# Kernel tuning notes

Measured on AMD Instinct MI355X. Metric: run time of the kernel, lower is better.

Reference implementation:

```python
import jax, jax.numpy as jnp
import numpy as np
import math

B, T, HID = 4, 1024, 1024
N_ATTN, N_HEAD, CTX = 1024, 64, 1024
HEAD_SIZE = N_ATTN // N_HEAD


def _make_time_w():
    ww = np.ones((N_HEAD, CTX), dtype=np.float32)
    curve = np.arange(CTX, dtype=np.float64) - (CTX - 1)  # -(CTX-1-i)
    for h in range(N_HEAD):
        decay = math.pow(CTX, -(h + 1) / (N_HEAD - 1)) if h < N_HEAD - 1 else 0.0
        ww[h] = np.exp(curve * decay).astype(np.float32)
    return jnp.asarray(ww)


def setup_inputs() -> dict:
    key = jax.random.key(0)
    ks = jax.random.split(key, 9)
    s = 0.02
    return {
        'x': jax.random.normal(ks[0], (B, T, HID), jnp.float32),
        'time_w': _make_time_w(),                                   # [H, CTX]
        'time_alpha': jnp.ones((N_HEAD, 1, CTX), jnp.float32),
        'time_beta': jnp.ones((N_HEAD, CTX, 1), jnp.float32),
        'time_gamma': jnp.ones((CTX, 1), jnp.float32),
        'Wk': jax.random.normal(ks[1], (HID, N_ATTN), jnp.float32) * s,
        'bk': jnp.zeros((N_ATTN,), jnp.float32),
        'Wv': jax.random.normal(ks[2], (HID, N_ATTN), jnp.float32) * s,
        'bv': jnp.zeros((N_ATTN,), jnp.float32),
        'Wr': jax.random.normal(ks[3], (HID, N_ATTN), jnp.float32) * s,
        'br': jnp.zeros((N_ATTN,), jnp.float32),
        'Wo': jax.random.normal(ks[4], (N_ATTN, HID), jnp.float32) * s,
        'bo': jnp.zeros((HID,), jnp.float32),
    }


def reference(x, time_w, time_alpha, time_beta, time_gamma, Wk, bk, Wv, bv, Wr, br, Wo, bo):
    Bn, Tn, C = x.shape
    H, TT = time_w.shape
    hs = N_ATTN // H
    # --- Toeplitz causal decay matrix: w[h,t,u] = time_w[h, TT-1-(t-u)] for u<=t else 0 ---
    t = jnp.arange(Tn)
    rel = (TT - 1) - t[:, None] + t[None, :]            # [T, T]
    mask = t[None, :] <= t[:, None]                     # u <= t (causal)
    w = jnp.where(mask[None], time_w[:, jnp.clip(rel, 0, TT - 1)], 0.0)  # [H, T, T]
    w = w * time_alpha[:, :, :Tn] * time_beta[:, :Tn, :]
    # --- half-channel time shift (shift first C//2 channels back by one step) ---
    half = x[:, :, : C // 2]
    shifted = jnp.concatenate([jnp.zeros_like(half[:, :1]), half[:, :-1]], axis=1)
    xs = jnp.concatenate([shifted, x[:, :, C // 2:]], axis=-1)
    # --- projections ---
    k = xs @ Wk + bk
    v = xs @ Wv + bv
    r = xs @ Wr + br
    k = jnp.exp(jnp.clip(k, -60.0, 30.0))
    sum_k = jnp.cumsum(k, axis=1)
    kv = (k * v).reshape(Bn, Tn, H, hs)
    wkv = jnp.einsum('htu,buhc->bthc', w, kv).reshape(Bn, Tn, -1)
    rwkv = jax.nn.sigmoid(r) * wkv / sum_k
    out = rwkv @ Wo + bo
    return out * time_gamma[:Tn]
```

## Files before the change

### kernel.cpp

```cpp
#include <hip/hip_runtime.h>
#include <hip/hip_bf16.h>
#include <cstddef>
#include <cstdint>

#define Bn   4
#define Tn   1024
#define HID  1024
#define NH   64
#define HS   16
#define NA   1024

typedef short v8s __attribute__((ext_vector_type(8)));
typedef float v4f __attribute__((ext_vector_type(4)));

typedef __attribute__((address_space(1))) void* as1_void;
typedef __attribute__((address_space(3))) void* as3_void;

__device__ __forceinline__ void gload_lds16(const void* g, void* l) {
    __builtin_amdgcn_global_load_lds((as1_void)(void*)g, (as3_void)l, 16, 0, 0);
}

__device__ __forceinline__ short f2bf(float f) {
    __hip_bfloat16 h = __float2bfloat16(f);
    return *reinterpret_cast<short*>(&h);
}
__device__ __forceinline__ float bf2f(short s) {
    __hip_bfloat16 h = *reinterpret_cast<__hip_bfloat16*>(&s);
    return __bfloat162float(h);
}

__global__ __launch_bounds__(256)
void prep(const float* __restrict__ x,
          const float* __restrict__ W0, const float* __restrict__ W1,
          const float* __restrict__ W2, const float* __restrict__ W3,
          short* __restrict__ xs, short* __restrict__ Wt)
{
    __shared__ float tile[32][33];
    const int bid = blockIdx.x;
    const int tid = threadIdx.x;
    if (bid < 4096) {
        int idx = bid * 256 + tid;
        int m  = idx >> 8;
        int c4 = (idx & 255) * 4;
        int t  = m & (Tn - 1);
        float4 v;
        if (c4 < HID / 2) {
            if (t == 0) v = make_float4(0.f, 0.f, 0.f, 0.f);
            else        v = *(const float4*)(x + (size_t)(m - 1) * HID + c4);
        } else {
            v = *(const float4*)(x + (size_t)m * HID + c4);
        }
        short4 o;
        o.x = f2bf(v.x); o.y = f2bf(v.y); o.z = f2bf(v.z); o.w = f2bf(v.w);
        *(short4*)(xs + (size_t)m * HID + c4) = o;
    } else {
        int b2 = bid - 4096;
        int z  = b2 >> 10;
        int rem = b2 & 1023;
        const float* W = (z == 0) ? W0 : (z == 1) ? W1 : (z == 2) ? W2 : W3;
        short* dst = Wt + (size_t)z * 1024 * 1024;
        int k0 = (rem & 31) * 32;
        int n0 = (rem >> 5) * 32;
        int tx = tid & 31;
        int ty = tid >> 5;
        #pragma unroll
        for (int j = 0; j < 4; ++j)
            tile[ty + 8 * j][tx] = W[(size_t)(k0 + ty + 8 * j) * NA + n0 + tx];
        __syncthreads();
        #pragma unroll
        for (int j = 0; j < 4; ++j)
            dst[(size_t)(n0 + ty + 8 * j) * HID + k0 + tx] = f2bf(tile[tx][ty + 8 * j]);
    }
}

template<int EPI, int TN>
__global__ __launch_bounds__(256)
void gemm_db(const short* __restrict__ A, const short* __restrict__ Bt,
             const float* __restrict__ b0, const float* __restrict__ b1,
             const float* __restrict__ b2,
             short* __restrict__ kout, short* __restrict__ vout,
             short* __restrict__ sout, float* __restrict__ fout,
             const float* __restrict__ gamma)
{
    constexpr int NT = TN / 32;
    constexpr int BI = TN / 64;
    constexpr int STAGE = 2 * 128 * 32 + 2 * TN * 32;
    constexpr int TILE  = (EPI == 0) ? 128 * 136 : 0;
    constexpr int SMEM  = STAGE > TILE ? STAGE : TILE;
    __shared__ short smem[SMEM];
    short* As = smem;
    short* Bs = smem + 2 * 128 * 32;

    const int tid  = threadIdx.x;
    const int wave = tid >> 6;
    const int lane = tid & 63;

    int id = blockIdx.x;
    int brow, bcol;
    if (TN == 128) { int grp = id / 192, l = id % 192; brow = grp * 8 + (l & 7); bcol = (l >> 3) % 24; }
    else           { int grp = id / 128, l = id % 128; brow = grp * 8 + (l & 7); bcol = l >> 3; }
    const int bm = brow * 128;
    const int bn = bcol * TN;

    const int wm = (wave & 1) * 64;
    const int wn = (wave >> 1) * (TN / 2);
    const int lm = lane & 15;
    const int lq = lane >> 4;
    const int lr = lane >> 2;
    const int l4 = lane & 3;

    v4f acc[4][NT];
    #pragma unroll
    for (int i = 0; i < 4; ++i)
        #pragma unroll
        for (int j = 0; j < NT; ++j) acc[i][j] = (v4f){0.f, 0.f, 0.f, 0.f};

    const short* ag[2];
    int adst[2];
    #pragma unroll
    for (int i = 0; i < 2; ++i) {
        int r = wave * 32 + i * 16 + lr;
        int q = (l4 - (r >> 1)) & 3;
        ag[i]  = A + (size_t)(bm + r) * 1024 + q * 8;
        adst[i] = (wave * 32 + i * 16) * 32;
    }
    const short* bg[BI];
    int bdst[BI];
    #pragma unroll
    for (int i = 0; i < BI; ++i) {
        int r = wave * (TN / 4) + i * 16 + lr;
        int q = (l4 - (r >> 1)) & 3;
        bg[i]  = Bt + (size_t)(bn + r) * 1024 + q * 8;
        bdst[i] = (wave * (TN / 4) + i * 16) * 32;
    }
    int afo[4], bfo[NT];
    #pragma unroll
    for (int t = 0; t < 4; ++t) {
        int r = wm + t * 16 + lm;
        afo[t] = r * 32 + (((lq + (r >> 1)) & 3)) * 8;
    }
    #pragma unroll
    for (int nt = 0; nt < NT; ++nt) {
        int r = wn + nt * 16 + lm;
        bfo[nt] = r * 32 + (((lq + (r >> 1)) & 3)) * 8;
    }

    #pragma unroll
    for (int i = 0; i < 2; ++i)  gload_lds16(ag[i],  &As[adst[i]]);
    #pragma unroll
    for (int i = 0; i < BI; ++i) gload_lds16(bg[i],  &Bs[bdst[i]]);

    #pragma unroll 2
    for (int it = 0; it < 32; ++it) {
        const int cur = it & 1;
        if (it < 31) {
            int k1 = (it + 1) * 32;
            int nxt = cur ^ 1;
            #pragma unroll
            for (int i = 0; i < 2; ++i)
                gload_lds16(ag[i] + k1, &As[nxt * 4096 + adst[i]]);
            #pragma unroll
            for (int i = 0; i < BI; ++i)
                gload_lds16(bg[i] + k1, &Bs[nxt * TN * 32 + bdst[i]]);
            asm volatile("s_waitcnt vmcnt(%0)" :: "i"(2 + BI) : "memory");
        } else {
            asm volatile("s_waitcnt vmcnt(0)" ::: "memory");
        }
        asm volatile("s_barrier" ::: "memory");

        v8s af[4], bfr[NT];
        #pragma unroll
        for (int t = 0; t < 4; ++t)
            af[t] = *(const v8s*)&As[cur * 4096 + afo[t]];
        #pragma unroll
        for (int nt = 0; nt < NT; ++nt)
            bfr[nt] = *(const v8s*)&Bs[cur * TN * 32 + bfo[nt]];
        #pragma unroll
        for (int mt = 0; mt < 4; ++mt)
            #pragma unroll
            for (int nt = 0; nt < NT; ++nt)
                acc[mt][nt] = __builtin_amdgcn_mfma_f32_16x16x32_bf16(
                    bfr[nt], af[mt], acc[mt][nt], 0, 0, 0);

        asm volatile("s_barrier" ::: "memory");
    }

    if (EPI == 0) {
        __syncthreads();
        short* tile = smem;
        const int type = bn >> 10;
        const int cb = bn & 1023;
        const float* bias = (type == 0) ? b0 : (type == 1) ? b1 : b2;
        #pragma unroll
        for (int mt = 0; mt < 4; ++mt) {
            int ml = wm + mt * 16 + lm;
            #pragma unroll
            for (int nt = 0; nt < NT; ++nt) {
                int nl = wn + nt * 16 + lq * 4;
                float4 bv4 = *(const float4*)&bias[cb + nl];
                short4 o;
                #pragma unroll
                for (int r = 0; r < 4; ++r) {
                    float v = acc[mt][nt][r] + ((const float*)&bv4)[r];
                    if (type == 0) {
                        v = fminf(fmaxf(v, -60.f), 30.f);
                        v = __expf(v);
                    } else if (type == 2) {
                        v = __builtin_amdgcn_rcpf(1.f + __expf(-v));
                    }
                    ((short*)&o)[r] = f2bf(v);
                }
                *(short4*)&tile[ml * 136 + nl] = o;
            }
        }
        __syncthreads();
        short* outp = (type == 0) ? kout : (type == 1) ? vout : sout;
        const int rml = tid >> 4;
        const int rnl = (tid & 15) * 8;
        #pragma unroll
        for (int p = 0; p < 8; ++p) {
            int ml = p * 16 + rml;
            int4 d = *(const int4*)&tile[ml * 136 + rnl];
            *(int4*)&outp[(size_t)(bm + ml) * 1024 + cb + rnl] = d;
        }
    } else {
        #pragma unroll
        for (int mt = 0; mt < 4; ++mt) {
            int m = bm + wm + mt * 16 + lm;
            float g = gamma[m & (Tn - 1)];
            #pragma unroll
            for (int nt = 0; nt < NT; ++nt) {
                int n0 = bn + wn + nt * 16 + lq * 4;
                float4 bv4 = *(const float4*)&b0[n0];
                float4 o;
                o.x = (acc[mt][nt][0] + bv4.x) * g;
                o.y = (acc[mt][nt][1] + bv4.y) * g;
                o.z = (acc[mt][nt][2] + bv4.z) * g;
                o.w = (acc[mt][nt][3] + bv4.w) * g;
                *(float4*)&fout[(size_t)m * 1024 + n0] = o;
            }
        }
    }
}

#define SEG 16
#define SEGL 64

__global__ __launch_bounds__(256)
void scan_passA(const short* __restrict__ kexp, const short* __restrict__ vbuf,
                const float* __restrict__ time_w, const float* __restrict__ alpha,
                float2* __restrict__ states)
{
    int gid = blockIdx.x * 256 + threadIdx.x;
    int c2  = (gid & 511) * 2;
    int b   = (gid >> 9) & 3;
    int seg = gid >> 11;
    int h   = c2 >> 4;
    float r = time_w[h * Tn + (Tn - 2)];
    int t0 = seg * SEGL;
    size_t base = ((size_t)(b * Tn + t0)) * NA + c2;
    const float* ap = alpha + h * Tn + t0;
    float S0 = 0.f, S1 = 0.f, ks0 = 0.f, ks1 = 0.f;
    #pragma unroll 4
    for (int i = 0; i < SEGL; ++i) {
        short2 kk = *(const short2*)(kexp + base + (size_t)i * NA);
        short2 vv = *(const short2*)(vbuf + base + (size_t)i * NA);
        float ke0 = bf2f(kk.x), ke1 = bf2f(kk.y);
        float a = ap[i];
        S0 = S0 * r + ke0 * bf2f(vv.x) * a;
        S1 = S1 * r + ke1 * bf2f(vv.y) * a;
        ks0 += ke0; ks1 += ke1;
    }
    int sidx = seg * 4096 + b * 1024 + c2;
    *(float4*)&states[sidx] = make_float4(S0, ks0, S1, ks1);
}

__global__ __launch_bounds__(256)
void scan_passC(const short* __restrict__ kexp, const short* __restrict__ vbuf,
                const short* __restrict__ sigr,
                const float* __restrict__ time_w, const float* __restrict__ alpha,
                const float* __restrict__ beta,
                const float2* __restrict__ states, short* __restrict__ out)
{
    int gid = blockIdx.x * 256 + threadIdx.x;
    int c2  = (gid & 511) * 2;
    int b   = (gid >> 9) & 3;
    int seg = gid >> 11;
    int h   = c2 >> 4;
    float r = time_w[h * Tn + (Tn - 2)];
    float rp = r;
    #pragma unroll
    for (int i = 0; i < 6; ++i) rp = rp * rp;
    float S0 = 0.f, ks0 = 0.f, S1 = 0.f, ks1 = 0.f;
    for (int s = 0; s < seg; ++s) {
        float2 st0 = states[s * 4096 + b * 1024 + c2];
        float2 st1 = states[s * 4096 + b * 1024 + c2 + 1];
        S0 = S0 * rp + st0.x;  ks0 += st0.y;
        S1 = S1 * rp + st1.x;  ks1 += st1.y;
    }
    int t0 = seg * SEGL;
    size_t base = ((size_t)(b * Tn + t0)) * NA + c2;
    const float* ap = alpha + h * Tn + t0;
    const float* bp = beta  + h * Tn + t0;
    #pragma unroll 4
    for (int i = 0; i < SEGL; ++i) {
        size_t idx = base + (size_t)i * NA;
        short2 kk = *(const short2*)(kexp + idx);
        short2 vv = *(const short2*)(vbuf + idx);
        short2 ss = *(const short2*)(sigr + idx);
        float a = ap[i], bt = bp[i];
        float ke0 = bf2f(kk.x), ke1 = bf2f(kk.y);
        S0 = S0 * r + ke0 * bf2f(vv.x) * a;
        S1 = S1 * r + ke1 * bf2f(vv.y) * a;
        ks0 += ke0; ks1 += ke1;
        short2 o;
        o.x = f2bf(bf2f(ss.x) * bt * S0 * __builtin_amdgcn_rcpf(ks0));
        o.y = f2bf(bf2f(ss.y) * bt * S1 * __builtin_amdgcn_rcpf(ks1));
        *(short2*)(out + idx) = o;
    }
}

extern "C" void kernel_launch(void* const* d_in, const int* in_sizes, int n_in,
                              void* d_out, int out_size, void* d_ws, size_t ws_size,
                              hipStream_t stream)
{
    const float* x      = (const float*)d_in[0];
    const float* time_w = (const float*)d_in[1];
    const float* alpha  = (const float*)d_in[2];
    const float* beta   = (const float*)d_in[3];
    const float* gamma  = (const float*)d_in[4];
    const float* Wk     = (const float*)d_in[5];
    const float* bk     = (const float*)d_in[6];
    const float* Wv     = (const float*)d_in[7];
    const float* bv     = (const float*)d_in[8];
    const float* Wr     = (const float*)d_in[9];
    const float* br     = (const float*)d_in[10];
    const float* Wo     = (const float*)d_in[11];
    const float* bo     = (const float*)d_in[12];
    float* out = (float*)d_out;

    char* ws = (char*)d_ws;

    short*  kbuf  = (short*)(ws);
    short*  vbuf  = (short*)(ws + ( 8u << 20));
    short*  sbuf  = (short*)(ws + (16u << 20));
    short*  xsbuf = (short*)(ws + (24u << 20));
    short*  Wt    = (short*)(ws + (32u << 20));
    float2* states= (float2*)(ws + (40u << 20));

    dim3 thr(256);

    prep<<<dim3(8192), thr, 0, stream>>>(x, Wk, Wv, Wr, Wo, xsbuf, Wt);

    gemm_db<0, 128><<<dim3(768), thr, 0, stream>>>(
        xsbuf, Wt, bk, bv, br, kbuf, vbuf, sbuf, nullptr, nullptr);

    scan_passA<<<dim3(128), thr, 0, stream>>>(kbuf, vbuf, time_w, alpha, states);
    scan_passC<<<dim3(128), thr, 0, stream>>>(kbuf, vbuf, sbuf,
                                              time_w, alpha, beta, states, xsbuf);

    gemm_db<1, 64><<<dim3(512), thr, 0, stream>>>(
        xsbuf, Wt + (size_t)3 * 1024 * 1024, bo, nullptr, nullptr,
        nullptr, nullptr, nullptr, out, gamma);
}
```

Measured before the change: 176.9 us.

## Triple-buffer GEMM LDS pipeline and double scan segment count

The GEMM main loop moves from a double-buffered LDS pipeline with two barriers per iteration to a three-stage ring that prefetches two K-steps ahead and needs only one barrier per iteration. Separately, the chunked scan uses 32 segments of length 32 instead of 16 of 64, launching twice as many blocks, and passC reads each segment state pair with one float4 load. The extra stage raises LDS use per block, which may reduce occupancy, and more segments lengthen passC's serial state prefix loop.

```diff
diff --git a/kernel.cpp b/kernel.cpp
--- a/kernel.cpp
+++ b/kernel.cpp
@@ -82,14 +82,13 @@
              short* __restrict__ sout, float* __restrict__ fout,
              const float* __restrict__ gamma)
 {
-    constexpr int NT = TN / 32;
-    constexpr int BI = TN / 64;
-    constexpr int STAGE = 2 * 128 * 32 + 2 * TN * 32;
-    constexpr int TILE  = (EPI == 0) ? 128 * 136 : 0;
-    constexpr int SMEM  = STAGE > TILE ? STAGE : TILE;
-    __shared__ short smem[SMEM];
-    short* As = smem;
-    short* Bs = smem + 2 * 128 * 32;
+    constexpr int NT  = TN / 32;
+    constexpr int BI  = TN / 64;
+    constexpr int SA  = 128 * 32;
+    constexpr int SB  = TN * 32;
+    constexpr int WAITN = 2 + BI;
+    __shared__ short As[3 * SA];
+    __shared__ short Bs[3 * SB];
 
     const int tid  = threadIdx.x;
     const int wave = tid >> 6;
@@ -137,44 +136,46 @@
     #pragma unroll
     for (int t = 0; t < 4; ++t) {
         int r = wm + t * 16 + lm;
-        afo[t] = r * 32 + (((lq + (r >> 1)) & 3)) * 8;
+        afo[t] = r * 32 + ((lq + (r >> 1)) & 3) * 8;
     }
     #pragma unroll
     for (int nt = 0; nt < NT; ++nt) {
         int r = wn + nt * 16 + lm;
-        bfo[nt] = r * 32 + (((lq + (r >> 1)) & 3)) * 8;
-    }
-
-    #pragma unroll
-    for (int i = 0; i < 2; ++i)  gload_lds16(ag[i],  &As[adst[i]]);
-    #pragma unroll
-    for (int i = 0; i < BI; ++i) gload_lds16(bg[i],  &Bs[bdst[i]]);
-
-    #pragma unroll 2
+        bfo[nt] = r * 32 + ((lq + (r >> 1)) & 3) * 8;
+    }
+
+    #pragma unroll
+    for (int s = 0; s < 2; ++s) {
+        int k = s * 32;
+        #pragma unroll
+        for (int i = 0; i < 2; ++i)  gload_lds16(ag[i] + k, &As[s * SA + adst[i]]);
+        #pragma unroll
+        for (int i = 0; i < BI; ++i) gload_lds16(bg[i] + k, &Bs[s * SB + bdst[i]]);
+    }
+
+    int coffA = 0, coffB = 0;
+    int poffA = 2 * SA, poffB = 2 * SB;
+
     for (int it = 0; it < 32; ++it) {
-        const int cur = it & 1;
-        if (it < 31) {
-            int k1 = (it + 1) * 32;
-            int nxt = cur ^ 1;
-            #pragma unroll
-            for (int i = 0; i < 2; ++i)
-                gload_lds16(ag[i] + k1, &As[nxt * 4096 + adst[i]]);
-            #pragma unroll
-            for (int i = 0; i < BI; ++i)
-                gload_lds16(bg[i] + k1, &Bs[nxt * TN * 32 + bdst[i]]);
-            asm volatile("s_waitcnt vmcnt(%0)" :: "i"(2 + BI) : "memory");
-        } else {
-            asm volatile("s_waitcnt vmcnt(0)" ::: "memory");
-        }
+        if (it < 31) asm volatile("s_waitcnt vmcnt(%0)" :: "i"(WAITN) : "memory");
+        else         asm volatile("s_waitcnt vmcnt(0)" ::: "memory");
         asm volatile("s_barrier" ::: "memory");
 
+        if (it < 30) {
+            int k2 = (it + 2) * 32;
+            #pragma unroll
+            for (int i = 0; i < 2; ++i)  gload_lds16(ag[i] + k2, &As[poffA + adst[i]]);
+            #pragma unroll
+            for (int i = 0; i < BI; ++i) gload_lds16(bg[i] + k2, &Bs[poffB + bdst[i]]);
+        }
+
         v8s af[4], bfr[NT];
         #pragma unroll
         for (int t = 0; t < 4; ++t)
-            af[t] = *(const v8s*)&As[cur * 4096 + afo[t]];
+            af[t] = *(const v8s*)&As[coffA + afo[t]];
         #pragma unroll
         for (int nt = 0; nt < NT; ++nt)
-            bfr[nt] = *(const v8s*)&Bs[cur * TN * 32 + bfo[nt]];
+            bfr[nt] = *(const v8s*)&Bs[coffB + bfo[nt]];
         #pragma unroll
         for (int mt = 0; mt < 4; ++mt)
             #pragma unroll
@@ -182,12 +183,15 @@
                 acc[mt][nt] = __builtin_amdgcn_mfma_f32_16x16x32_bf16(
                     bfr[nt], af[mt], acc[mt][nt], 0, 0, 0);
 
-        asm volatile("s_barrier" ::: "memory");
+        coffA += SA; if (coffA == 3 * SA) coffA = 0;
+        coffB += SB; if (coffB == 3 * SB) coffB = 0;
+        poffA += SA; if (poffA == 3 * SA) poffA = 0;
+        poffB += SB; if (poffB == 3 * SB) poffB = 0;
     }
 
     if (EPI == 0) {
         __syncthreads();
-        short* tile = smem;
+        short* tile = As;
         const int type = bn >> 10;
         const int cb = bn & 1023;
         const float* bias = (type == 0) ? b0 : (type == 1) ? b1 : b2;
@@ -243,8 +247,8 @@
     }
 }
 
-#define SEG 16
-#define SEGL 64
+#define SEG 32
+#define SEGL 32
 
 __global__ __launch_bounds__(256)
 void scan_passA(const short* __restrict__ kexp, const short* __restrict__ vbuf,
@@ -290,13 +294,12 @@
     float r = time_w[h * Tn + (Tn - 2)];
     float rp = r;
     #pragma unroll
-    for (int i = 0; i < 6; ++i) rp = rp * rp;
+    for (int i = 0; i < 5; ++i) rp = rp * rp;
     float S0 = 0.f, ks0 = 0.f, S1 = 0.f, ks1 = 0.f;
     for (int s = 0; s < seg; ++s) {
-        float2 st0 = states[s * 4096 + b * 1024 + c2];
-        float2 st1 = states[s * 4096 + b * 1024 + c2 + 1];
-        S0 = S0 * rp + st0.x;  ks0 += st0.y;
-        S1 = S1 * rp + st1.x;  ks1 += st1.y;
+        float4 st = *(const float4*)&states[s * 4096 + b * 1024 + c2];
+        S0 = S0 * rp + st.x;  ks0 += st.y;
+        S1 = S1 * rp + st.z;  ks1 += st.w;
     }
     int t0 = seg * SEGL;
     size_t base = ((size_t)(b * Tn + t0)) * NA + c2;
@@ -355,8 +358,8 @@
     gemm_db<0, 128><<<dim3(768), thr, 0, stream>>>(
         xsbuf, Wt, bk, bv, br, kbuf, vbuf, sbuf, nullptr, nullptr);
 
-    scan_passA<<<dim3(128), thr, 0, stream>>>(kbuf, vbuf, time_w, alpha, states);
-    scan_passC<<<dim3(128), thr, 0, stream>>>(kbuf, vbuf, sbuf,
+    scan_passA<<<dim3(256), thr, 0, stream>>>(kbuf, vbuf, time_w, alpha, states);
+    scan_passC<<<dim3(256), thr, 0, stream>>>(kbuf, vbuf, sbuf,
                                               time_w, alpha, beta, states, xsbuf);
 
     gemm_db<1, 64><<<dim3(512), thr, 0, stream>>>(
```

New measurement: 177.5 us. About the same (+0.3%).
